# Kernel optimization log

Measured on AMD Instinct MI355X. Metric: run time of the kernel, lower is better.

## Reference

```python
import jax, jax.numpy as jnp
import numpy as np

NUM_CLASSES = 80
NUM_TOP_QUERIES = 300
MASK_THRESHOLD = 0.5
OUT_SIZE = 480  # fixed original image size (all orig_target_sizes == 480)


def setup_inputs() -> dict:
    key = jax.random.key(0)
    k1, k2, k3 = jax.random.split(key, 3)
    B, Q, C, Hm, Wm = 2, 300, NUM_CLASSES, 128, 128
    pred_logits = jax.random.normal(k1, (B, Q, C), dtype=jnp.float32)
    pred_boxes = jax.random.uniform(k2, (B, Q, 4), dtype=jnp.float32)  # cxcywh in [0,1]
    pred_masks = jax.random.normal(k3, (B, Q, Hm, Wm), dtype=jnp.float32)
    orig_target_sizes = jnp.ones((B, 2), dtype=jnp.float32) * OUT_SIZE
    return {
        'pred_logits': pred_logits,
        'pred_boxes': pred_boxes,
        'pred_masks': pred_masks,
        'orig_target_sizes': orig_target_sizes,
    }


def _box_cxcywh_to_xyxy(boxes):
    cx, cy, w, h = jnp.split(boxes, 4, axis=-1)
    return jnp.concatenate([cx - 0.5 * w, cy - 0.5 * h, cx + 0.5 * w, cy + 0.5 * h], axis=-1)


def reference(pred_logits, pred_boxes, pred_masks, orig_target_sizes):
    B, Q, C = pred_logits.shape
    Hm, Wm = pred_masks.shape[-2:]
    K = NUM_TOP_QUERIES

    # box conversion + scaling to original image size ([s0,s1,s0,s1] like repeat(1,2))
    scale = jnp.tile(orig_target_sizes, (1, 2))[:, None, :]  # [B,1,4]
    scaled_boxes = _box_cxcywh_to_xyxy(pred_boxes) * scale    # [B,Q,4]

    # focal-loss path: sigmoid scores, flattened top-k over (Q*C)
    scores = jax.nn.sigmoid(pred_logits).reshape(B, Q * C)
    top_scores, top_indices = jax.lax.top_k(scores, K)        # [B,K]
    top_labels = top_indices % C
    query_indices = top_indices // C                          # [B,K]

    selected_boxes = jnp.take_along_axis(scaled_boxes, query_indices[..., None], axis=1)  # [B,K,4]

    # per-sample mask selection + sigmoid + bilinear upsample (align_corners=False)
    sel_masks = jnp.take_along_axis(pred_masks, query_indices[..., None, None], axis=1)   # [B,K,Hm,Wm]
    mask_probs = jax.nn.sigmoid(sel_masks)
    up = jax.vmap(lambda m: jax.image.resize(m, (OUT_SIZE, OUT_SIZE), 'bilinear'))(
        mask_probs.reshape(B * K, Hm, Wm)
    ).reshape(B, K, OUT_SIZE, OUT_SIZE)
    binary_masks = up > MASK_THRESHOLD                        # [B,K,H,W] bool (torch adds channel dim of 1)

    return top_scores, top_labels, selected_boxes, binary_masks
```

## Files before the change

### kernel.cpp

```cpp
#include <hip/hip_runtime.h>
#include <math.h>

#define BATCH 2
#define NQ    300
#define NC    80
#define NFLAT (NQ * NC)
#define TOPK  300
#define HM    128
#define OUTS  480
#define NBKT  4096
#define CAP   4096

#define INVSCALE  (128.0 / 480.0)
#define INVSCALEF 0.26666668f

typedef float v4f __attribute__((ext_vector_type(4)));

__device__ __forceinline__ unsigned mapf(float x) {
    unsigned u = __float_as_uint(x);
    return (u & 0x80000000u) ? ~u : (u | 0x80000000u);
}

__global__ __launch_bounds__(1024) void topk_kernel(
    const float* __restrict__ logits,
    const float* __restrict__ boxes,
    const float* __restrict__ osize,
    float* __restrict__ out,
    int* __restrict__ qidx)
{
    __shared__ unsigned hist[NBKT];
    __shared__ unsigned long long cand[CAP];
    __shared__ unsigned psum[1024];
    __shared__ unsigned sh_T;
    __shared__ unsigned sh_cnt;

    const int b = blockIdx.x;
    const int tid = threadIdx.x;
    const float* lg = logits + (size_t)b * NFLAT;

    for (int i = tid; i < NBKT; i += 1024) hist[i] = 0;
    if (tid == 0) sh_cnt = 0;
    __syncthreads();
    for (int i = tid; i < NFLAT; i += 1024)
        atomicAdd(&hist[mapf(lg[i]) >> 20], 1u);
    __syncthreads();

    unsigned gsum = hist[4 * tid] + hist[4 * tid + 1] + hist[4 * tid + 2] + hist[4 * tid + 3];
    psum[tid] = gsum;
    __syncthreads();
    for (unsigned off = 1; off < 1024; off <<= 1) {
        unsigned v = (tid + off < 1024) ? psum[tid + off] : 0u;
        __syncthreads();
        psum[tid] += v;
        __syncthreads();
    }
    {
        unsigned nxt = (tid == 1023) ? 0u : psum[tid + 1];
        if (psum[tid] >= (unsigned)TOPK && nxt < (unsigned)TOPK) {
            unsigned acc = nxt, T = 4u * (unsigned)tid;
            for (int bk = 4 * tid + 3; bk >= 4 * tid; --bk) {
                if (acc + hist[bk] >= (unsigned)TOPK) { T = (unsigned)bk; break; }
                acc += hist[bk];
            }
            sh_T = T;
        }
    }
    __syncthreads();
    const unsigned T = sh_T;

    for (int i = tid; i < NFLAT; i += 1024) {
        unsigned m = mapf(lg[i]);
        if ((m >> 20) >= T) {
            unsigned pos = atomicAdd(&sh_cnt, 1u);
            if (pos < CAP)
                cand[pos] = ((unsigned long long)m << 32)
                          | (unsigned long long)(0xFFFFFFFFu - (unsigned)i);
        }
    }
    __syncthreads();
    const unsigned cnt = (sh_cnt > CAP) ? CAP : sh_cnt;

    for (unsigned t = tid; t < cnt; t += 1024) {
        const unsigned long long my = cand[t];
        unsigned rank = 0;
        for (unsigned j = 0; j < cnt; ++j) rank += (cand[j] > my) ? 1u : 0u;
        if (rank < (unsigned)TOPK) {
            unsigned idx = 0xFFFFFFFFu - (unsigned)(my & 0xFFFFFFFFull);
            int q = (int)(idx / NC);
            int c = (int)(idx % NC);
            double x = (double)lg[idx];
            double score = 1.0 / (1.0 + exp(-x));

            out[b * TOPK + rank] = (float)score;
            out[BATCH * TOPK + b * TOPK + rank] = (float)c;

            const float* bx = boxes + ((size_t)(b * NQ + q)) * 4;
            double cx = (double)bx[0], cy = (double)bx[1];
            double w  = (double)bx[2], h  = (double)bx[3];
            double s0 = (double)osize[b * 2 + 0];
            double s1 = (double)osize[b * 2 + 1];
            float* ob = out + 2 * BATCH * TOPK + ((size_t)(b * TOPK + rank)) * 4;
            ob[0] = (float)((cx - 0.5 * w) * s0);
            ob[1] = (float)((cy - 0.5 * h) * s1);
            ob[2] = (float)((cx + 0.5 * w) * s0);
            ob[3] = (float)((cy + 0.5 * h) * s1);

            qidx[b * TOPK + rank] = q;
        }
    }
}

#define VROWS   16
#define NVS     (OUTS / VROWS)
#define MAXR    6

__global__ __launch_bounds__(256) void mask_kernel(
    const float* __restrict__ masks,
    const int* __restrict__ qidx,
    float* __restrict__ outm)
{
    __shared__ float sig[MAXR * HM];

    const int tid = threadIdx.x;
    const int unit = blockIdx.x;
    const int mask_id = unit / NVS;
    const int vs = unit % NVS;
    const int ys = vs * VROWS;
    const int b = mask_id / TOPK;
    const int q = qidx[mask_id];

    float s_first = ((float)ys + 0.5f) * INVSCALEF - 0.5f;
    float s_last  = ((float)(ys + VROWS - 1) + 0.5f) * INVSCALEF - 0.5f;
    int r_lo = (int)floorf(s_first);
    if (r_lo < 0) r_lo = 0; if (r_lo > HM - 2) r_lo = HM - 2;
    int r_hi = (int)floorf(s_last);
    if (r_hi < 0) r_hi = 0; if (r_hi > HM - 2) r_hi = HM - 2;
    r_hi += 1;
    const int cnt = r_hi - r_lo + 1;

    const v4f* s4 = (const v4f*)(masks
                      + ((size_t)(b * NQ + q)) * (HM * HM)
                      + (size_t)r_lo * HM);
    const int n4 = cnt * (HM / 4);
    if (tid < n4) {
        v4f v = s4[tid];
        float* dst = sig + tid * 4;
        dst[0] = 1.0f / (1.0f + __expf(-v.x));
        dst[1] = 1.0f / (1.0f + __expf(-v.y));
        dst[2] = 1.0f / (1.0f + __expf(-v.z));
        dst[3] = 1.0f / (1.0f + __expf(-v.w));
    }

    const int qd = tid % 120;
    const int yy = tid / 120;
    const int x0 = qd * 4;
    int c0 = 0, ar[4];
    float fxr[4];
    #pragma unroll
    for (int j = 0; j < 4; ++j) {
        float sx = ((float)(x0 + j) + 0.5f) * INVSCALEF - 0.5f;
        int jx = (int)floorf(sx);
        if (jx < 0) jx = 0; if (jx > HM - 2) jx = HM - 2;
        float f = sx - (float)jx;
        f = fminf(fmaxf(f, 0.0f), 1.0f);
        if (j == 0) c0 = jx;
        ar[j]  = jx - c0;
        fxr[j] = f;
    }
    const int c1 = c0 + 1;
    const int c2 = (c0 + 2 > HM - 1) ? (HM - 1) : (c0 + 2);

    __syncthreads();

    if (tid < 240) {
        float* outp = outm + (size_t)mask_id * (OUTS * OUTS)
                           + (size_t)(ys + yy) * OUTS + x0;
        #pragma unroll
        for (int it = 0; it < VROWS / 2; ++it) {
            const int y = ys + yy + it * 2;
            float sy = ((float)y + 0.5f) * INVSCALEF - 0.5f;
            int jy = (int)floorf(sy);
            if (jy < 0) jy = 0; if (jy > HM - 2) jy = HM - 2;
            float fy = sy - (float)jy;
            fy = fminf(fmaxf(fy, 0.0f), 1.0f);

            const float* r0 = sig + (size_t)(jy - r_lo) * HM;
            const float* r1 = r0 + HM;
            const float wy1 = fy, wy0 = 1.0f - fy;

            const float t0 = wy0 * r0[c0] + wy1 * r1[c0];
            const float t1 = wy0 * r0[c1] + wy1 * r1[c1];
            const float t2 = wy0 * r0[c2] + wy1 * r1[c2];

            v4f res;
            #pragma unroll
            for (int j = 0; j < 4; ++j) {
                const float ta = ar[j] ? t1 : t0;
                const float tb = ar[j] ? t2 : t1;
                const float val = ta + fxr[j] * (tb - ta);
                res[j] = (val > 0.5f) ? 1.0f : 0.0f;
            }
            *((v4f*)(outp + (size_t)(it * 2) * OUTS)) = res;
        }
    }
}

extern "C" void kernel_launch(void* const* d_in, const int* in_sizes, int n_in,
                              void* d_out, int out_size, void* d_ws, size_t ws_size,
                              hipStream_t stream) {
    const float* logits = (const float*)d_in[0];
    const float* boxes  = (const float*)d_in[1];
    const float* masks  = (const float*)d_in[2];
    const float* osize  = (const float*)d_in[3];
    float* out = (float*)d_out;
    int* qidx = (int*)d_ws;

    topk_kernel<<<BATCH, 1024, 0, stream>>>(logits, boxes, osize, out, qidx);

    mask_kernel<<<BATCH * TOPK * NVS, 256, 0, stream>>>(masks, qidx, out + 3600);
}
```

Measured before the change: 149.9 us.

## Split top-k histogram into a multi-block kernel before selection

Moves the per-batch score histogram out of the two-block top-k kernel into a separate kernel that uses 8 blocks per batch, each building a partial histogram in shared memory and writing it to workspace. The select kernel then sums the partial histograms instead of reading all logits with shared atomics. This spreads the histogram pass across more compute units, at the cost of an extra launch and a global round trip for 16 histograms.

```diff
diff --git a/kernel.cpp b/kernel.cpp
--- a/kernel.cpp
+++ b/kernel.cpp
@@ -11,7 +11,10 @@
 #define NBKT  4096
 #define CAP   4096
 
-#define INVSCALE  (128.0 / 480.0)
+#define HBLK  8
+#define HTHR  512
+#define CHUNK (NFLAT / HBLK)
+
 #define INVSCALEF 0.26666668f
 
 typedef float v4f __attribute__((ext_vector_type(4)));
@@ -21,10 +24,29 @@
     return (u & 0x80000000u) ? ~u : (u | 0x80000000u);
 }
 
-__global__ __launch_bounds__(1024) void topk_kernel(
+__global__ __launch_bounds__(HTHR) void hist_kernel(
+    const float* __restrict__ logits,
+    unsigned* __restrict__ ghist)
+{
+    __shared__ unsigned h[NBKT];
+    const int blk = blockIdx.x;
+    const int b = blk / HBLK, sub = blk % HBLK;
+    const float* lg = logits + (size_t)b * NFLAT + (size_t)sub * CHUNK;
+
+    for (int i = threadIdx.x; i < NBKT; i += HTHR) h[i] = 0;
+    __syncthreads();
+    for (int i = threadIdx.x; i < CHUNK; i += HTHR)
+        atomicAdd(&h[mapf(lg[i]) >> 20], 1u);
+    __syncthreads();
+    unsigned* dst = ghist + (size_t)blk * NBKT;
+    for (int i = threadIdx.x; i < NBKT; i += HTHR) dst[i] = h[i];
+}
+
+__global__ __launch_bounds__(1024) void select_kernel(
     const float* __restrict__ logits,
     const float* __restrict__ boxes,
     const float* __restrict__ osize,
+    const unsigned* __restrict__ ghist,
     float* __restrict__ out,
     int* __restrict__ qidx)
 {
@@ -38,15 +60,17 @@
     const int tid = threadIdx.x;
     const float* lg = logits + (size_t)b * NFLAT;
 
-    for (int i = tid; i < NBKT; i += 1024) hist[i] = 0;
+    for (int i = tid; i < NBKT; i += 1024) {
+        unsigned s = 0;
+        #pragma unroll
+        for (int k = 0; k < HBLK; ++k)
+            s += ghist[(size_t)(b * HBLK + k) * NBKT + i];
+        hist[i] = s;
+    }
     if (tid == 0) sh_cnt = 0;
     __syncthreads();
-    for (int i = tid; i < NFLAT; i += 1024)
-        atomicAdd(&hist[mapf(lg[i]) >> 20], 1u);
-    __syncthreads();
-
-    unsigned gsum = hist[4 * tid] + hist[4 * tid + 1] + hist[4 * tid + 2] + hist[4 * tid + 3];
-    psum[tid] = gsum;
+
+    psum[tid] = hist[4 * tid] + hist[4 * tid + 1] + hist[4 * tid + 2] + hist[4 * tid + 3];
     __syncthreads();
     for (unsigned off = 1; off < 1024; off <<= 1) {
         unsigned v = (tid + off < 1024) ? psum[tid + off] : 0u;
@@ -213,9 +237,12 @@
     const float* masks  = (const float*)d_in[2];
     const float* osize  = (const float*)d_in[3];
     float* out = (float*)d_out;
+
     int* qidx = (int*)d_ws;
-
-    topk_kernel<<<BATCH, 1024, 0, stream>>>(logits, boxes, osize, out, qidx);
+    unsigned* ghist = (unsigned*)((char*)d_ws + 4096);
+
+    hist_kernel<<<BATCH * HBLK, HTHR, 0, stream>>>(logits, ghist);
+    select_kernel<<<BATCH, 1024, 0, stream>>>(logits, boxes, osize, ghist, out, qidx);
 
     mask_kernel<<<BATCH * TOPK * NVS, 256, 0, stream>>>(masks, qidx, out + 3600);
 }
```

Result: no change. 149.1 us (-0.6%).
